# Performance work log

Hardware: AMD Instinct MI355X
Metric: run time of the kernel (lower is better)

## Reference

```python
import jax, jax.numpy as jnp
import numpy as np

NEG = 0.01   # LeakyReLU slope (torch default)
EPS = 1e-5   # BatchNorm1d eps

def lrelu(x):
    return jnp.where(x >= 0, x, NEG * x)

def bn(x, g, b):
    # BatchNorm1d in training mode: biased batch stats
    m = x.mean(0)
    v = x.var(0)
    return g * (x - m) * jax.lax.rsqrt(v + EPS) + b

def gcn_conv(x, edge_index, edge_weight, W, b):
    # PyG GCNConv: add self-loops (weight 1), symmetric normalization, X W then aggregate
    N = x.shape[0]
    loop = jnp.arange(N)
    src = jnp.concatenate([edge_index[0], loop])
    dst = jnp.concatenate([edge_index[1], loop])
    w = jnp.concatenate([edge_weight, jnp.ones((N,), x.dtype)])
    deg = jax.ops.segment_sum(w, dst, num_segments=N)
    dinv = jnp.where(deg > 0, jax.lax.rsqrt(deg), 0.0)
    norm = dinv[src] * w * dinv[dst]            # [E+N]
    h = x @ W                                   # [N, out]
    out = jax.ops.segment_sum(norm[:, None] * h[src], dst, num_segments=N)
    return out + b


def setup_inputs() -> dict:
    key = jax.random.key(0)
    ks = iter(jax.random.split(key, 48))
    B, Nd, Ed, Np_, Ep = 2048, 10000, 65536, 5000, 25000
    D_IN, P_IN, F = 1024, 2812, 300 + 1024 + 1024 + 1024  # F = 3372

    def w(shape):
        return (jax.random.normal(next(ks), shape, jnp.float32) * 0.02)

    inp = {
        'd_index': jax.random.randint(next(ks), (B,), 0, Nd),
        'p_index': jax.random.randint(next(ks), (B,), 0, Np_),
        'd_vecs': jax.random.normal(next(ks), (B, 300), jnp.float32),
        'p_embeddings': jax.random.normal(next(ks), (B, 1024), jnp.float32),
        'd_ecfps': jax.random.normal(next(ks), (Nd, D_IN), jnp.float32),
        'd_edge_index': jax.random.randint(next(ks), (2, Ed), 0, Nd),
        'd_edge_weight': jax.random.uniform(next(ks), (Ed,), jnp.float32),
        'p_gos': jax.random.normal(next(ks), (Np_, P_IN), jnp.float32),
        'p_edge_index': jax.random.randint(next(ks), (2, Ep), 0, Np_),
        'p_edge_weight': jax.random.uniform(next(ks), (Ep,), jnp.float32),
        # GCN params
        'd_gcn_W': w((D_IN, 1024)), 'd_gcn_b': jnp.zeros((1024,), jnp.float32),
        'p_gcn_W': w((P_IN, 1024)), 'p_gcn_b': jnp.zeros((1024,), jnp.float32),
        # encoder
        'enc_W1': w((F, 1024)), 'enc_b1': jnp.zeros((1024,), jnp.float32),
        'enc_g1': jnp.ones((1024,), jnp.float32), 'enc_beta1': jnp.zeros((1024,), jnp.float32),
        'enc_W2': w((1024, 256)), 'enc_b2': jnp.zeros((256,), jnp.float32),
        'enc_g2': jnp.ones((256,), jnp.float32), 'enc_beta2': jnp.zeros((256,), jnp.float32),
        # decoder
        'dec_W1': w((256, 1024)), 'dec_b1': jnp.zeros((1024,), jnp.float32),
        'dec_g1': jnp.ones((1024,), jnp.float32), 'dec_beta1': jnp.zeros((1024,), jnp.float32),
        'dec_W2': w((1024, F)), 'dec_b2': jnp.zeros((F,), jnp.float32),
        'dec_g2': jnp.ones((F,), jnp.float32), 'dec_beta2': jnp.zeros((F,), jnp.float32),
        # output head
        'out_W1': w((256, 64)), 'out_b1': jnp.zeros((64,), jnp.float32),
        'out_g1': jnp.ones((64,), jnp.float32), 'out_beta1': jnp.zeros((64,), jnp.float32),
        'out_W2': w((64, 1)), 'out_b2': jnp.zeros((1,), jnp.float32),
    }
    return inp


def reference(d_index, p_index, d_vecs, p_embeddings, d_ecfps, d_edge_index, d_edge_weight,
              p_gos, p_edge_index, p_edge_weight,
              d_gcn_W, d_gcn_b, p_gcn_W, p_gcn_b,
              enc_W1, enc_b1, enc_g1, enc_beta1, enc_W2, enc_b2, enc_g2, enc_beta2,
              dec_W1, dec_b1, dec_g1, dec_beta1, dec_W2, dec_b2, dec_g2, dec_beta2,
              out_W1, out_b1, out_g1, out_beta1, out_W2, out_b2):
    ecfps = lrelu(gcn_conv(d_ecfps, d_edge_index, d_edge_weight, d_gcn_W, d_gcn_b))[d_index]
    gos = lrelu(gcn_conv(p_gos, p_edge_index, p_edge_weight, p_gcn_W, p_gcn_b))[p_index]
    feature = jnp.concatenate([d_vecs, p_embeddings, ecfps, gos], axis=1)  # [B, 3372]
    h = jax.nn.relu(bn(feature @ enc_W1 + enc_b1, enc_g1, enc_beta1))
    encoded = jax.nn.relu(bn(h @ enc_W2 + enc_b2, enc_g2, enc_beta2))       # [B, 256]
    h = jax.nn.relu(bn(encoded @ dec_W1 + dec_b1, dec_g1, dec_beta1))
    decoded = jax.nn.relu(bn(h @ dec_W2 + dec_b2, dec_g2, dec_beta2))       # [B, 3372]
    h = lrelu(bn(encoded @ out_W1 + out_b1, out_g1, out_beta1))
    y = h @ out_W2 + out_b2                                                  # [B, 1]
    return (y, encoded, decoded, feature)
```

## Files before the change

kernel.cpp:

```cpp
#include <hip/hip_runtime.h>

#define CDIV(a,b) (((a)+(b)-1)/(b))

typedef __attribute__((ext_vector_type(8))) short bf16x8;
typedef __attribute__((ext_vector_type(4))) float f32x4;

__device__ __forceinline__ unsigned short f2b(float v) {
  union { float f; unsigned u; } x; x.f = v;
  unsigned r = x.u + 0x7FFFu + ((x.u >> 16) & 1u);
  return (unsigned short)(r >> 16);
}

__device__ __forceinline__ void gload_lds16(const void* g, void* l) {
  __builtin_amdgcn_global_load_lds(
      (const __attribute__((address_space(1))) unsigned int*)(g),
      (__attribute__((address_space(3))) unsigned int*)(l), 16, 0, 0);
}

struct GA {
  const unsigned short* A;
  const unsigned short* B;
  float* C;
  const int* ridx;
  float* csum;
  float* csumsq;
  int N, K, lda, ldb;
};

__global__ __launch_bounds__(256) void gemm128z(GA g0, GA g1, GA g2, GA g3) {
  __shared__ __align__(16) unsigned short As[2][128 * 64];
  __shared__ __align__(16) unsigned short Bs[2][128 * 64];
  const int z = blockIdx.z;
  GA g = (z == 0) ? g0 : (z == 1) ? g1 : (z == 2) ? g2 : g3;

  const int tid = threadIdx.x;
  const int lane = tid & 63;
  const int wid = tid >> 6;
  const int wm = (wid >> 1) * 64;
  const int wn = (wid & 1) * 64;
  const long bm = (long)blockIdx.x * 128;
  const long bn = (long)blockIdx.y * 128;

  f32x4 acc[4][4] = {};

  const int lr = tid >> 3;
  const int lc = (((tid & 7) ^ (lr & 7)) * 8);

  const unsigned short* ap[4];
  const unsigned short* bp[4];
#pragma unroll
  for (int i = 0; i < 4; ++i) {
    long row = bm + i * 32 + lr;
    long arow = g.ridx ? (long)g.ridx[row] : row;
    ap[i] = g.A + arow * g.lda + lc;
    bp[i] = g.B + (bn + i * 32 + lr) * (long)g.ldb + lc;
  }

  const int rsel = lane & 15;
  const int rx = rsel & 7;

  auto STAGE = [&](int buf, int k0) {
#pragma unroll
    for (int i = 0; i < 4; ++i) {
      const int eoff = (i * 256 + tid) * 8;
      gload_lds16(ap[i] + k0, &As[buf][eoff]);
      gload_lds16(bp[i] + k0, &Bs[buf][eoff]);
    }
  };
  auto COMPUTE = [&](int buf) {
#pragma unroll
    for (int kk = 0; kk < 2; ++kk) {
      const int koz = (((kk * 4 + (lane >> 4)) ^ rx) << 3);
      bf16x8 av[4], bv[4];
#pragma unroll
      for (int m = 0; m < 4; ++m)
        av[m] = *(const bf16x8*)(&As[buf][(wm + m * 16 + rsel) * 64 + koz]);
#pragma unroll
      for (int n = 0; n < 4; ++n)
        bv[n] = *(const bf16x8*)(&Bs[buf][(wn + n * 16 + rsel) * 64 + koz]);
#pragma unroll
      for (int m = 0; m < 4; ++m)
#pragma unroll
        for (int n = 0; n < 4; ++n)
          acc[m][n] = __builtin_amdgcn_mfma_f32_16x16x32_bf16(av[m], bv[n], acc[m][n], 0, 0, 0);
    }
  };

  STAGE(0, 0);
  int cur = 0;
  for (int k0 = 64; k0 < g.K; k0 += 64) {
    STAGE(cur ^ 1, k0);
    asm volatile("s_waitcnt vmcnt(8)" ::: "memory");
    __builtin_amdgcn_s_barrier();
    asm volatile("" ::: "memory");
    COMPUTE(cur);
    asm volatile("" ::: "memory");
    __builtin_amdgcn_s_barrier();
    cur ^= 1;
  }
  asm volatile("s_waitcnt vmcnt(0)" ::: "memory");
  __builtin_amdgcn_s_barrier();
  asm volatile("" ::: "memory");
  COMPUTE(cur);

  const int crow0 = (lane >> 4) * 4;
  const int ccol = lane & 15;
#pragma unroll
  for (int m = 0; m < 4; ++m)
#pragma unroll
    for (int n = 0; n < 4; ++n) {
      const long r = bm + wm + m * 16 + crow0;
      const long c = bn + wn + n * 16 + ccol;
#pragma unroll
      for (int q = 0; q < 4; ++q)
        g.C[(r + q) * (long)g.N + c] = acc[m][n][q];
    }

  if (g.csum) {
#pragma unroll
    for (int n = 0; n < 4; ++n) {
      float s = 0.f, s2 = 0.f;
#pragma unroll
      for (int m = 0; m < 4; ++m)
#pragma unroll
        for (int q = 0; q < 4; ++q) {
          float v = acc[m][n][q];
          s += v; s2 += v * v;
        }
      s  += __shfl_xor(s, 16);  s  += __shfl_xor(s, 32);
      s2 += __shfl_xor(s2, 16); s2 += __shfl_xor(s2, 32);
      if ((lane >> 4) == 0) {
        const long c = bn + wn + n * 16 + ccol;
        atomicAdd(&g.csum[c], s);
        atomicAdd(&g.csumsq[c], s2);
      }
    }
  }
}

__global__ __launch_bounds__(256) void gemm64s(GA g0, GA g1, GA g2, GA g3) {
  __shared__ __align__(16) unsigned short As[2][64 * 64];
  __shared__ __align__(16) unsigned short Bs[2][128 * 64];
  const int z = blockIdx.z;
  GA g = (z == 0) ? g0 : (z == 1) ? g1 : (z == 2) ? g2 : g3;

  const int tid = threadIdx.x;
  const int lane = tid & 63;
  const int wid = tid >> 6;
  const int wn = wid * 32;
  const long bm = (long)blockIdx.x * 64;
  const long bn = (long)blockIdx.y * 128;

  f32x4 acc[4][2] = {};

  const int lr = tid >> 3;
  const int lc = (((tid & 7) ^ (lr & 7)) * 8);

  const long r0 = g.ridx ? (long)g.ridx[bm + lr] : bm + lr;
  const long r1 = g.ridx ? (long)g.ridx[bm + 32 + lr] : bm + 32 + lr;
  const unsigned short* ap0 = g.A + r0 * g.lda + lc;
  const unsigned short* ap1 = g.A + r1 * g.lda + lc;
  const unsigned short* bp0 = g.B + (bn + lr) * (long)g.ldb + lc;
  const unsigned short* bp1 = g.B + (bn + 32 + lr) * (long)g.ldb + lc;
  const unsigned short* bp2 = g.B + (bn + 64 + lr) * (long)g.ldb + lc;
  const unsigned short* bp3 = g.B + (bn + 96 + lr) * (long)g.ldb + lc;

  const int rsel = lane & 15;
  const int rx = rsel & 7;

  auto STAGE = [&](int buf, int k0) {
    gload_lds16(ap0 + k0, &As[buf][tid * 8]);
    gload_lds16(ap1 + k0, &As[buf][(256 + tid) * 8]);
    gload_lds16(bp0 + k0, &Bs[buf][tid * 8]);
    gload_lds16(bp1 + k0, &Bs[buf][(256 + tid) * 8]);
    gload_lds16(bp2 + k0, &Bs[buf][(512 + tid) * 8]);
    gload_lds16(bp3 + k0, &Bs[buf][(768 + tid) * 8]);
  };
  auto COMPUTE = [&](int buf) {
#pragma unroll
    for (int kk = 0; kk < 2; ++kk) {
      const int koz = (((kk * 4 + (lane >> 4)) ^ rx) << 3);
      bf16x8 av[4], bv[2];
#pragma unroll
      for (int m = 0; m < 4; ++m)
        av[m] = *(const bf16x8*)(&As[buf][(m * 16 + rsel) * 64 + koz]);
#pragma unroll
      for (int n = 0; n < 2; ++n)
        bv[n] = *(const bf16x8*)(&Bs[buf][(wn + n * 16 + rsel) * 64 + koz]);
#pragma unroll
      for (int m = 0; m < 4; ++m)
#pragma unroll
        for (int n = 0; n < 2; ++n)
          acc[m][n] = __builtin_amdgcn_mfma_f32_16x16x32_bf16(av[m], bv[n], acc[m][n], 0, 0, 0);
    }
  };

  STAGE(0, 0);
  int cur = 0;
  for (int k0 = 64; k0 < g.K; k0 += 64) {
    STAGE(cur ^ 1, k0);
    asm volatile("s_waitcnt vmcnt(6)" ::: "memory");
    __builtin_amdgcn_s_barrier();
    asm volatile("" ::: "memory");
    COMPUTE(cur);
    asm volatile("" ::: "memory");
    __builtin_amdgcn_s_barrier();
    cur ^= 1;
  }
  asm volatile("s_waitcnt vmcnt(0)" ::: "memory");
  __builtin_amdgcn_s_barrier();
  asm volatile("" ::: "memory");
  COMPUTE(cur);

  const int crow0 = (lane >> 4) * 4;
  const int ccol = lane & 15;
#pragma unroll
  for (int m = 0; m < 4; ++m)
#pragma unroll
    for (int n = 0; n < 2; ++n) {
      const long r = bm + m * 16 + crow0;
      const long c = bn + wn + n * 16 + ccol;
#pragma unroll
      for (int q = 0; q < 4; ++q)
        g.C[(r + q) * (long)g.N + c] = acc[m][n][q];
    }

  if (g.csum) {
#pragma unroll
    for (int n = 0; n < 2; ++n) {
      float s = 0.f, s2 = 0.f;
#pragma unroll
      for (int m = 0; m < 4; ++m)
#pragma unroll
        for (int q = 0; q < 4; ++q) {
          float v = acc[m][n][q];
          s += v; s2 += v * v;
        }
      s  += __shfl_xor(s, 16);  s  += __shfl_xor(s, 32);
      s2 += __shfl_xor(s2, 16); s2 += __shfl_xor(s2, 32);
      if ((lane >> 4) == 0) {
        const long c = bn + wn + n * 16 + ccol;
        atomicAdd(&g.csum[c], s);
        atomicAdd(&g.csumsq[c], s2);
      }
    }
  }
}

__global__ void init_all(int* iz, int nIz, float* deg, int nDeg,
                         float* stats, int nStats) {
  int i = blockIdx.x * 256 + threadIdx.x;
  if (i < nIz) iz[i] = 0;
  if (i < nDeg) deg[i] = 1.f;
  if (i < nStats) stats[i] = 0.f;
}

__global__ void prep_b(const int* __restrict__ d_ei, const float* __restrict__ d_ew,
                       float* __restrict__ deg_d,
                       const int* __restrict__ p_ei, const float* __restrict__ p_ew,
                       float* __restrict__ deg_p,
                       const int* __restrict__ d_index, int* __restrict__ flag_d,
                       const int* __restrict__ p_index, int* __restrict__ flag_p) {
  int e = blockIdx.x * 256 + threadIdx.x;
  if (e < 65536) atomicAdd(&deg_d[d_ei[65536 + e]], d_ew[e]);
  int e2 = e - 65536;
  if (e2 >= 0 && e2 < 25000) atomicAdd(&deg_p[p_ei[25000 + e2]], p_ew[e2]);
  if (e < 2048) flag_d[d_index[e]] = 1;
  else if (e < 4096) flag_p[p_index[e - 2048]] = 1;
}

__global__ void prep_c(float* __restrict__ deg, int nDeg,
                       int* __restrict__ flag_d, int* __restrict__ ctr_d,
                       int* __restrict__ slot_d,
                       int* __restrict__ flag_p, int* __restrict__ ctr_p,
                       int* __restrict__ slot_p) {
  int i = blockIdx.x * 256 + threadIdx.x;
  if (i < nDeg) deg[i] = rsqrtf(deg[i]);
  if (i < 10000) {
    if (flag_d[i]) { int s = atomicAdd(ctr_d, 1); flag_d[i] = s + 1; slot_d[s] = i; }
  } else if (i < 15000) {
    int j = i - 10000;
    if (flag_p[j]) { int s = atomicAdd(ctr_p, 1); flag_p[j] = s + 1; slot_p[s] = j; }
  }
}

__global__ void prep_d(const int* __restrict__ d_index, const int* __restrict__ flag_d,
                       int* __restrict__ ridx_d,
                       const int* __restrict__ p_index, const int* __restrict__ flag_p,
                       int* __restrict__ ridx_p,
                       const int* __restrict__ d_ei, int* __restrict__ cnt_d,
                       const int* __restrict__ p_ei, int* __restrict__ cnt_p) {
  int e = blockIdx.x * 256 + threadIdx.x;
  if (e < 2048) ridx_d[e] = flag_d[d_index[e]] - 1;
  else if (e < 4096) { int j = e - 2048; ridx_p[j] = flag_p[p_index[j]] - 1; }
  if (e < 65536) { int s = flag_d[d_ei[65536 + e]]; if (s) atomicAdd(&cnt_d[s - 1], 1); }
  int e2 = e - 65536;
  if (e2 >= 0 && e2 < 25000) { int s = flag_p[p_ei[25000 + e2]]; if (s) atomicAdd(&cnt_p[s - 1], 1); }
}

__global__ void scan2048x2(const int* __restrict__ cnt_d, int* __restrict__ rp_d,
                           const int* __restrict__ cnt_p, int* __restrict__ rp_p) {
  const int* cnt = blockIdx.x ? cnt_p : cnt_d;
  int* rowptr    = blockIdx.x ? rp_p : rp_d;
  __shared__ int part[256];
  int tid = threadIdx.x;
  int base = tid * 8;
  int vals[8]; int s = 0;
#pragma unroll
  for (int i = 0; i < 8; ++i) { vals[i] = s; s += cnt[base + i]; }
  part[tid] = s;
  __syncthreads();
  if (tid == 0) { int r = 0; for (int i = 0; i < 256; ++i) { int t = part[i]; part[i] = r; r += t; } }
  __syncthreads();
  int off = part[tid];
#pragma unroll
  for (int i = 0; i < 8; ++i) rowptr[base + i] = off + vals[i];
  if (tid == 255) rowptr[2048] = off + s;
}
__global__ void fill_edges2(
    const int* __restrict__ d_ei, const float* __restrict__ d_ew,
    const float* __restrict__ dinv_d, const int* __restrict__ flag_d,
    const int* __restrict__ rp_d, int* __restrict__ fill_d,
    int2* __restrict__ em_d,
    const int* __restrict__ p_ei, const float* __restrict__ p_ew,
    const float* __restrict__ dinv_p, const int* __restrict__ flag_p,
    const int* __restrict__ rp_p, int* __restrict__ fill_p,
    int2* __restrict__ em_p) {
  int e = blockIdx.x * 256 + threadIdx.x;
  if (e < 65536) {
    int dst = d_ei[65536 + e];
    int s = flag_d[dst];
    if (s) {
      int src = d_ei[e];
      int pos = rp_d[s - 1] + atomicAdd(&fill_d[s - 1], 1);
      float cf = d_ew[e] * dinv_d[src] * dinv_d[dst];
      em_d[pos] = make_int2(src, __float_as_int(cf));
    }
  }
  int e2 = e - 65536;
  if (e2 >= 0 && e2 < 25000) {
    int dst = p_ei[25000 + e2];
    int s = flag_p[dst];
    if (s) {
      int src = p_ei[e2];
      int pos = rp_p[s - 1] + atomicAdd(&fill_p[s - 1], 1);
      float cf = p_ew[e2] * dinv_p[src] * dinv_p[dst];
      em_p[pos] = make_int2(src, __float_as_int(cf));
    }
  }
}

__global__ __launch_bounds__(256) void gather_agg5b(
    const float* __restrict__ Xd, const float* __restrict__ dinv_d,
    const int* __restrict__ slot_d, const int* __restrict__ rp_d,
    const int2* __restrict__ em_d,
    const int* __restrict__ nflag_d, unsigned short* __restrict__ aggd,
    const float* __restrict__ Xp, const float* __restrict__ dinv_p,
    const int* __restrict__ slot_p, const int* __restrict__ rp_p,
    const int2* __restrict__ em_p,
    const int* __restrict__ nflag_p, unsigned short* __restrict__ aggp)
{
  const int gw = blockIdx.x * 4 + (threadIdx.x >> 6);
  const int lane = threadIdx.x & 63;

  int slot, c, Kdata4, Kst4, Kld, nflag;
  const float *X, *dinv; const int *slotn, *rp; const int2* em;
  unsigned short* agg;
  if (gw < 8192) {
    slot = gw >> 2;
    c = (gw & 3) * 64 + lane;
    X = Xd; dinv = dinv_d; slotn = slot_d; rp = rp_d; em = em_d;
    nflag = *nflag_d; agg = aggd; Kdata4 = 256; Kst4 = 256; Kld = 1024;
  } else {
    int q = gw - 8192;
    slot = q / 11;
    c = (q - slot * 11) * 64 + lane;
    X = Xp; dinv = dinv_p; slotn = slot_p; rp = rp_p; em = em_p;
    nflag = *nflag_p; agg = aggp; Kdata4 = 703; Kst4 = 704; Kld = 2812;
  }
  if (slot >= nflag) return;

  const int n = slotn[slot];
  const float dn = dinv[n];
  const float selfc = dn * dn;
  const int e0 = rp[slot], e1 = rp[slot + 1];
  const bool valid = c < Kdata4;

  float ax = 0.f, ay = 0.f, az = 0.f, aw = 0.f;
  if (valid) {
    float4 v = *(const float4*)(X + (long)n * Kld + 4 * c);
    ax = selfc * v.x; ay = selfc * v.y; az = selfc * v.z; aw = selfc * v.w;
  }

  int e = e0;
  for (; e + 4 <= e1; e += 4) {
    const int2 m0 = em[e], m1 = em[e + 1], m2 = em[e + 2], m3 = em[e + 3];
    if (valid) {
      float4 v0 = *(const float4*)(X + (long)m0.x * Kld + 4 * c);
      float4 v1 = *(const float4*)(X + (long)m1.x * Kld + 4 * c);
      float4 v2 = *(const float4*)(X + (long)m2.x * Kld + 4 * c);
      float4 v3 = *(const float4*)(X + (long)m3.x * Kld + 4 * c);
      const float c0 = __int_as_float(m0.y), c1 = __int_as_float(m1.y);
      const float c2 = __int_as_float(m2.y), c3 = __int_as_float(m3.y);
      ax += c0 * v0.x; ay += c0 * v0.y; az += c0 * v0.z; aw += c0 * v0.w;
      ax += c1 * v1.x; ay += c1 * v1.y; az += c1 * v1.z; aw += c1 * v1.w;
      ax += c2 * v2.x; ay += c2 * v2.y; az += c2 * v2.z; aw += c2 * v2.w;
      ax += c3 * v3.x; ay += c3 * v3.y; az += c3 * v3.z; aw += c3 * v3.w;
    }
  }
  for (; e < e1; ++e) {
    const int2 m = em[e];
    if (valid) {
      float4 v = *(const float4*)(X + (long)m.x * Kld + 4 * c);
      const float cf = __int_as_float(m.y);
      ax += cf * v.x; ay += cf * v.y; az += cf * v.z; aw += cf * v.w;
    }
  }

  if (c < Kst4) {
    ushort4 o; o.x = f2b(ax); o.y = f2b(ay); o.z = f2b(az); o.w = f2b(aw);
    *(ushort4*)(agg + (long)slot * (Kst4 * 4) + 4 * c) = o;
  }
}

__global__ void transposeAll(
    const float* W0, unsigned short* T0,
    const float* W1, unsigned short* T1,
    const float* W2, unsigned short* T2,
    const float* W3, unsigned short* T3,
    const float* W4, unsigned short* T4,
    const float* W5, unsigned short* T5,
    const float* W6, unsigned short* T6)
{
  __shared__ float tile[32][33];
  int bid = blockIdx.x;
  const float* W; unsigned short* Wt; int K, N, Kp, Np_, tx, local;
  if      (bid <  1024) { W=W0; Wt=T0; K=1024; N=1024; Kp=1024; Np_=1024; tx=32;  local=bid; }
  else if (bid <  3840) { W=W1; Wt=T1; K=2812; N=1024; Kp=2816; Np_=1024; tx=88;  local=bid-1024; }
  else if (bid <  7296) { W=W2; Wt=T2; K=3372; N=1024; Kp=3456; Np_=1024; tx=108; local=bid-3840; }
  else if (bid <  7552) { W=W3; Wt=T3; K=1024; N=256;  Kp=1024; Np_=256;  tx=32;  local=bid-7296; }
  else if (bid <  7808) { W=W4; Wt=T4; K=256;  N=1024; Kp=256;  Np_=1024; tx=8;   local=bid-7552; }
  else if (bid <  7840) { W=W5; Wt=T5; K=256;  N=64;   Kp=256;  Np_=128;  tx=8;   local=bid-7808; }
  else                  { W=W6; Wt=T6; K=1024; N=3372; Kp=1024; Np_=3456; tx=32;  local=bid-7840; }
  int k0 = (local % tx) * 32, n0 = (local / tx) * 32;
  for (int i = threadIdx.y; i < 32; i += 8) {
    int k = k0 + i, n = n0 + threadIdx.x;
    tile[i][threadIdx.x] = (k < K && n < N) ? W[(size_t)k * N + n] : 0.f;
  }
  __syncthreads();
  for (int i = threadIdx.y; i < 32; i += 8) {
    int n = n0 + i, k = k0 + threadIdx.x;
    if (n < Np_ && k < Kp) Wt[(size_t)n * Kp + k] = f2b(tile[threadIdx.x][i]);
  }
}

__global__ void colstats4(const float* __restrict__ Z, const float* __restrict__ Z2,
                          const float* __restrict__ Z3, int ldz, int cols,
                          float* __restrict__ csum, float* __restrict__ csumsq) {
  int c4 = blockIdx.x * 256 + threadIdx.x;
  if (c4 * 4 >= cols) return;
  int r0 = blockIdx.y * 16;
  float sx = 0.f, sy = 0.f, sz_ = 0.f, sw = 0.f;
  float qx = 0.f, qy = 0.f, qz = 0.f, qw = 0.f;
  for (int r = r0; r < r0 + 16; ++r) {
    float4 v = *(const float4*)(Z + (long)r * ldz + 4 * c4);
    if (Z2) { float4 w = *(const float4*)(Z2 + (long)r * ldz + 4 * c4);
              v.x += w.x; v.y += w.y; v.z += w.z; v.w += w.w; }
    if (Z3) { float4 w = *(const float4*)(Z3 + (long)r * ldz + 4 * c4);
              v.x += w.x; v.y += w.y; v.z += w.z; v.w += w.w; }
    sx += v.x; sy += v.y; sz_ += v.z; sw += v.w;
    qx += v.x * v.x; qy += v.y * v.y; qz += v.z * v.z; qw += v.w * v.w;
  }
  atomicAdd(&csum[4 * c4 + 0], sx); atomicAdd(&csum[4 * c4 + 1], sy);
  atomicAdd(&csum[4 * c4 + 2], sz_); atomicAdd(&csum[4 * c4 + 3], sw);
  atomicAdd(&csumsq[4 * c4 + 0], qx); atomicAdd(&csumsq[4 * c4 + 1], qy);
  atomicAdd(&csumsq[4 * c4 + 2], qz); atomicAdd(&csumsq[4 * c4 + 3], qw);
}

__global__ void apply_bn4(const float* __restrict__ Z, const float* __restrict__ Z2,
                          const float* __restrict__ Z3,
                          int ldz, int total4, int cols4,
                          const float* __restrict__ csum, const float* __restrict__ csumsq,
                          const float* __restrict__ g, const float* __restrict__ beta,
                          int leaky,
                          float* __restrict__ f32out, int ldf,
                          unsigned short* __restrict__ b16out, int ldb) {
  int idx = blockIdx.x*256+threadIdx.x;
  if (idx >= total4) return;
  int b = idx / cols4, j = (idx % cols4) * 4;
  float4 v = *(const float4*)(Z + (long)b * ldz + j);
  if (Z2) { float4 w = *(const float4*)(Z2 + (long)b * ldz + j);
            v.x += w.x; v.y += w.y; v.z += w.z; v.w += w.w; }
  if (Z3) { float4 w = *(const float4*)(Z3 + (long)b * ldz + j);
            v.x += w.x; v.y += w.y; v.z += w.z; v.w += w.w; }
  if (csum) {
    const float invB = 1.f / 2048.f;
    float4 cs = *(const float4*)(csum + j);
    float4 cq = *(const float4*)(csumsq + j);
    float4 gg = *(const float4*)(g + j);
    float4 bb = *(const float4*)(beta + j);
    float m, var, sc;
    m = cs.x * invB; var = fmaxf(cq.x * invB - m * m, 0.f);
    sc = gg.x * rsqrtf(var + 1e-5f); v.x = v.x * sc + (bb.x - m * sc);
    m = cs.y * invB; var = fmaxf(cq.y * invB - m * m, 0.f);
    sc = gg.y * rsqrtf(var + 1e-5f); v.y = v.y * sc + (bb.y - m * sc);
    m = cs.z * invB; var = fmaxf(cq.z * invB - m * m, 0.f);
    sc = gg.z * rsqrtf(var + 1e-5f); v.z = v.z * sc + (bb.z - m * sc);
    m = cs.w * invB; var = fmaxf(cq.w * invB - m * m, 0.f);
    sc = gg.w * rsqrtf(var + 1e-5f); v.w = v.w * sc + (bb.w - m * sc);
  } else {
    float4 bb = *(const float4*)(beta + j);
    v.x += bb.x; v.y += bb.y; v.z += bb.z; v.w += bb.w;
  }
  const float neg = leaky ? 0.01f : 0.f;
  v.x = (v.x >= 0.f) ? v.x : neg * v.x;
  v.y = (v.y >= 0.f) ? v.y : neg * v.y;
  v.z = (v.z >= 0.f) ? v.z : neg * v.z;
  v.w = (v.w >= 0.f) ? v.w : neg * v.w;
  if (f32out) *(float4*)(f32out + (long)b * ldf + j) = v;
  if (b16out) {
    ushort4 o; o.x = f2b(v.x); o.y = f2b(v.y); o.z = f2b(v.z); o.w = f2b(v.w);
    *(ushort4*)(b16out + (long)b * ldb + j) = o;
  }
}

__global__ void apply_gcn2(const float* __restrict__ Zd, const float* __restrict__ Pd,
                           const float* __restrict__ bd,
                           const float* __restrict__ Zp, const float* __restrict__ Pp,
                           const float* __restrict__ bp,
                           float* __restrict__ feat_f32, unsigned short* __restrict__ feat_b16) {
  int idx = blockIdx.x*256+threadIdx.x;
  if (idx >= 2 * 2048 * 256) return;
  const bool isP = idx >= 2048 * 256;
  int l = isP ? idx - 2048 * 256 : idx;
  int b = l >> 8, j = (l & 255) * 4;
  const float* Z = isP ? Zp : Zd;
  const float* P = isP ? Pp : Pd;
  const float* bias = isP ? bp : bd;
  const int coloff = isP ? 2348 : 1324;
  float4 v = *(const float4*)(Z + (long)b * 1024 + j);
  float4 w = *(const float4*)(P + (long)b * 1024 + j);
  float4 bb = *(const float4*)(bias + j);
  v.x += w.x + bb.x; v.y += w.y + bb.y; v.z += w.z + bb.z; v.w += w.w + bb.w;
  v.x = (v.x >= 0.f) ? v.x : 0.01f * v.x;
  v.y = (v.y >= 0.f) ? v.y : 0.01f * v.y;
  v.z = (v.z >= 0.f) ? v.z : 0.01f * v.z;
  v.w = (v.w >= 0.f) ? v.w : 0.01f * v.w;
  *(float4*)(feat_f32 + (long)b * 3372 + coloff + j) = v;
  ushort4 o; o.x = f2b(v.x); o.y = f2b(v.y); o.z = f2b(v.z); o.w = f2b(v.w);
  *(ushort4*)(feat_b16 + (long)b * 3456 + coloff + j) = o;
}

__global__ void feat_copy2(const float* __restrict__ dv, const float* __restrict__ pe,
                           float* __restrict__ f32out, unsigned short* __restrict__ b16out) {
  int idx = blockIdx.x*256+threadIdx.x;
  if (idx >= 2048 * 1408) return;
  int b = idx / 1408, c = idx % 1408;
  if (c < 1324) {
    float v = (c < 300) ? dv[b * 300 + c] : pe[(long)b * 1024 + (c - 300)];
    f32out[(long)b * 3372 + c] = v;
    b16out[(long)b * 3456 + c] = f2b(v);
  } else {
    b16out[(long)b * 3456 + 3372 + (c - 1324)] = 0;
  }
}

__global__ void head_fused(const float* __restrict__ Z, int ldz,
                           const float* __restrict__ csum, const float* __restrict__ csumsq,
                           const float* __restrict__ g, const float* __restrict__ beta,
                           const float* __restrict__ W2, const float* __restrict__ b2,
                           float* __restrict__ y) {
  int b = blockIdx.x*256+threadIdx.x;
  if (b >= 2048) return;
  const float invB = 1.f / 2048.f;
  float s = b2[0];
  for (int k = 0; k < 64; ++k) {
    float m = csum[k] * invB;
    float var = fmaxf(csumsq[k] * invB - m * m, 0.f);
    float sc = g[k] * rsqrtf(var + 1e-5f);
    float sh = beta[k] - m * sc;
    float v = Z[(long)b * ldz + k];
    v = v * sc + sh;
    v = (v >= 0.f) ? v : 0.01f * v;
    s += v * W2[k];
  }
  y[b] = s;
}

extern "C" void kernel_launch(void* const* d_in, const int* in_sizes, int n_in,
                              void* d_out, int out_size, void* d_ws, size_t ws_size,
                              hipStream_t stream) {
  (void)in_sizes; (void)n_in; (void)out_size; (void)ws_size;
  const int*   d_index = (const int*)d_in[0];
  const int*   p_index = (const int*)d_in[1];
  const float* d_vecs  = (const float*)d_in[2];
  const float* p_emb   = (const float*)d_in[3];
  const float* d_ecfps = (const float*)d_in[4];
  const int*   d_ei    = (const int*)d_in[5];
  const float* d_ew    = (const float*)d_in[6];
  const float* p_gos   = (const float*)d_in[7];
  const int*   p_ei    = (const int*)d_in[8];
  const float* p_ew    = (const float*)d_in[9];
  const float* d_gcn_W = (const float*)d_in[10];
  const float* d_gcn_b = (const float*)d_in[11];
  const float* p_gcn_W = (const float*)d_in[12];
  const float* p_gcn_b = (const float*)d_in[13];
  const float* enc_W1  = (const float*)d_in[14];
  const float* enc_g1  = (const float*)d_in[16];
  const float* enc_be1 = (const float*)d_in[17];
  const float* enc_W2  = (const float*)d_in[18];
  const float* enc_g2  = (const float*)d_in[20];
  const float* enc_be2 = (const float*)d_in[21];
  const float* dec_W1  = (const float*)d_in[22];
  const float* dec_g1  = (const float*)d_in[24];
  const float* dec_be1 = (const float*)d_in[25];
  const float* dec_W2  = (const float*)d_in[26];
  const float* dec_g2  = (const float*)d_in[28];
  const float* dec_be2 = (const float*)d_in[29];
  const float* out_W1  = (const float*)d_in[30];
  const float* out_g1  = (const float*)d_in[32];
  const float* out_be1 = (const float*)d_in[33];
  const float* out_W2  = (const float*)d_in[34];
  const float* out_b2  = (const float*)d_in[35];

  float* out = (float*)d_out;
  float* y_out    = out;
  float* enc_out  = out + 2048;
  float* dec_out  = out + 526336;
  float* feat_out = out + 7432192;

  char* ws = (char*)d_ws;
  size_t off = 0;
  auto alloc = [&](size_t bytes) {
    size_t o = off; off = (off + bytes + 255) & ~(size_t)255; return (void*)(ws + o);
  };
  int* iz = (int*)alloc((size_t)23194 * 4);
  int* flag_d = iz;
  int* flag_p = iz + 10000;
  int* cnt_d  = iz + 15000;
  int* cnt_p  = iz + 17048;
  int* fill_d = iz + 19096;
  int* fill_p = iz + 21144;
  int* ctr    = iz + 23192;
  int* slotnode_d = (int*)alloc(2048 * 4);
  int* slotnode_p = (int*)alloc(2048 * 4);
  int* rowptr_d = (int*)alloc(2049 * 4);
  int* rowptr_p = (int*)alloc(2049 * 4);
  int* ridx_d = (int*)alloc(2048 * 4);
  int* ridx_p = (int*)alloc(2048 * 4);
  int2* em_d = (int2*)alloc((size_t)65536 * 8);
  int2* em_p = (int2*)alloc((size_t)25000 * 8);
  float* deg   = (float*)alloc((size_t)15000 * 4);
  float* deg_d = deg;
  float* deg_p = deg + 10000;
  float* stats = (float*)alloc((size_t)34560 * 4);
  float* cs_e1 = stats,         * cq_e1 = stats + 3456;
  float* cs_e2 = stats + 6912,  * cq_e2 = stats + 10368;
  float* cs_d1 = stats + 13824, * cq_d1 = stats + 17280;
  float* cs_d2 = stats + 27648, * cq_d2 = stats + 31104;
  unsigned short* aggd_b = (unsigned short*)alloc((size_t)2048 * 1024 * 2);
  unsigned short* aggp_b = (unsigned short*)alloc((size_t)2048 * 2816 * 2);
  unsigned short* WdT   = (unsigned short*)alloc((size_t)1024 * 1024 * 2);
  unsigned short* WpT   = (unsigned short*)alloc((size_t)1024 * 2816 * 2);
  unsigned short* eW1T  = (unsigned short*)alloc((size_t)1024 * 3456 * 2);
  unsigned short* eW2T  = (unsigned short*)alloc((size_t)256 * 1024 * 2);
  unsigned short* dhT   = (unsigned short*)alloc((size_t)1152 * 256 * 2);
  unsigned short* dW2T  = (unsigned short*)alloc((size_t)3456 * 1024 * 2);
  unsigned short* featb = (unsigned short*)alloc((size_t)2048 * 3456 * 2);
  float* Z    = (float*)alloc((size_t)2048 * 3456 * 4);
  float* P0   = (float*)alloc((size_t)2048 * 1152 * 4);
  float* P1   = (float*)alloc((size_t)2048 * 1152 * 4);
  float* P2   = (float*)alloc((size_t)2048 * 1152 * 4);
  unsigned short* h1b  = (unsigned short*)alloc((size_t)2048 * 1024 * 2);
  unsigned short* encb = (unsigned short*)alloc((size_t)2048 * 256 * 2);
  unsigned short* h3b  = (unsigned short*)alloc((size_t)2048 * 1024 * 2);

  init_all<<<CDIV(34560,256),256,0,stream>>>(iz, 23194, deg, 15000, stats, 34560);
  prep_b<<<CDIV(90536,256),256,0,stream>>>(d_ei, d_ew, deg_d, p_ei, p_ew, deg_p,
                                           d_index, flag_d, p_index, flag_p);
  prep_c<<<CDIV(15000,256),256,0,stream>>>(deg, 15000, flag_d, ctr, slotnode_d,
                                           flag_p, ctr + 1, slotnode_p);
  prep_d<<<CDIV(90536,256),256,0,stream>>>(d_index, flag_d, ridx_d, p_index, flag_p, ridx_p,
                                           d_ei, cnt_d, p_ei, cnt_p);
  scan2048x2<<<2,256,0,stream>>>(cnt_d, rowptr_d, cnt_p, rowptr_p);
  fill_edges2<<<CDIV(90536,256),256,0,stream>>>(
      d_ei, d_ew, deg_d, flag_d, rowptr_d, fill_d, em_d,
      p_ei, p_ew, deg_p, flag_p, rowptr_p, fill_p, em_p);
  gather_agg5b<<<7680,256,0,stream>>>(
      d_ecfps, deg_d, slotnode_d, rowptr_d, em_d, ctr, aggd_b,
      p_gos,   deg_p, slotnode_p, rowptr_p, em_p, ctr + 1, aggp_b);

  transposeAll<<<11296, dim3(32,8), 0, stream>>>(
      d_gcn_W, WdT, p_gcn_W, WpT, enc_W1, eW1T, enc_W2, eW2T,
      dec_W1, dhT, out_W1, dhT + (size_t)1024 * 256, dec_W2, dW2T);

  {
    GA gd0{aggd_b,        WdT,        Z,  ridx_d, nullptr, nullptr, 1024,  512, 1024, 1024};
    GA gd1{aggd_b + 512,  WdT + 512,  P0, ridx_d, nullptr, nullptr, 1024,  512, 1024, 1024};
    GA gp0{aggp_b,        WpT,        P1, ridx_p, nullptr, nullptr, 1024, 1408, 2816, 2816};
    GA gp1{aggp_b + 1408, WpT + 1408, P2, ridx_p, nullptr, nullptr, 1024, 1408, 2816, 2816};
    gemm128z<<<dim3(16,8,4),256,0,stream>>>(gd0, gd1, gp0, gp1);
  }
  apply_gcn2<<<CDIV(2*2048*256,256),256,0,stream>>>(Z, P0, d_gcn_b, P1, P2, p_gcn_b,
                                                    feat_out, featb);
  feat_copy2<<<CDIV(2048*1408,256),256,0,stream>>>(d_vecs, p_emb, feat_out, featb);

  {
    GA e0{featb,        eW1T,        Z,  nullptr, nullptr, nullptr, 1024, 1152, 3456, 3456};
    GA e1{featb + 1152, eW1T + 1152, P0, nullptr, nullptr, nullptr, 1024, 1152, 3456, 3456};
    GA e2{featb + 2304, eW1T + 2304, P1, nullptr, nullptr, nullptr, 1024, 1152, 3456, 3456};
    gemm128z<<<dim3(16,8,3),256,0,stream>>>(e0, e1, e2, e0);
  }
  colstats4<<<dim3(1,128),256,0,stream>>>(Z, P0, P1, 1024, 1024, cs_e1, cq_e1);
  apply_bn4<<<CDIV(2048*256,256),256,0,stream>>>(Z, P0, P1, 1024, 2048*256, 256,
      cs_e1, cq_e1, enc_g1, enc_be1, 0, nullptr, 0, h1b, 1024);

  {
    GA e0{h1b,       eW2T,       Z,  nullptr, nullptr, nullptr, 256, 512, 1024, 1024};
    GA e1{h1b + 512, eW2T + 512, P0, nullptr, nullptr, nullptr, 256, 512, 1024, 1024};
    gemm64s<<<dim3(32,2,2),256,0,stream>>>(e0, e1, e0, e0);
  }
  colstats4<<<dim3(1,128),256,0,stream>>>(Z, P0, nullptr, 256, 256, cs_e2, cq_e2);
  apply_bn4<<<CDIV(2048*64,256),256,0,stream>>>(Z, P0, nullptr, 256, 2048*64, 64,
      cs_e2, cq_e2, enc_g2, enc_be2, 0, enc_out, 256, encb, 256);

  {
    GA g0{encb, dhT, Z, nullptr, cs_d1, cq_d1, 1152, 256, 256, 256};
    gemm64s<<<dim3(32,9,1),256,0,stream>>>(g0, g0, g0, g0);
  }
  apply_bn4<<<CDIV(2048*256,256),256,0,stream>>>(Z, nullptr, nullptr, 1152, 2048*256, 256,
      cs_d1, cq_d1, dec_g1, dec_be1, 0, nullptr, 0, h3b, 1024);
  head_fused<<<8,256,0,stream>>>(Z + 1024, 1152, cs_d1 + 1024, cq_d1 + 1024,
                                 out_g1, out_be1, out_W2, out_b2, y_out);

  {
    GA g0{h3b, dW2T, Z, nullptr, cs_d2, cq_d2, 3456, 1024, 1024, 1024};
    gemm128z<<<dim3(16,27,1),256,0,stream>>>(g0, g0, g0, g0);
  }
  apply_bn4<<<CDIV(2048*843,256),256,0,stream>>>(Z, nullptr, nullptr, 3456, 2048*843, 843,
      cs_d2, cq_d2, dec_g2, dec_be2, 0, dec_out, 3372, nullptr, 0);
}
```

Baseline: 291.0 us.

## Fuse final decoder GEMM with batchnorm via grid barrier; merge feature kernels

The last decoder GEMM now computes column statistics, waits at a global atomic-counter barrier until all 432 blocks finish, then applies batchnorm and ReLU straight from registers into the output. This drops the fp32 intermediate write and reread plus a separate apply_bn launch. The two feature-assembly kernels are also merged into one vectorized kernel. The grid barrier depends on all 432 blocks being co-resident, and the epilogue writes are strided per column (uncoalesced).

```diff
diff --git a/kernel.cpp b/kernel.cpp
--- a/kernel.cpp
+++ b/kernel.cpp
@@ -133,6 +133,138 @@
         const long c = bn + wn + n * 16 + ccol;
         atomicAdd(&g.csum[c], s);
         atomicAdd(&g.csumsq[c], s2);
+      }
+    }
+  }
+}
+
+__global__ __launch_bounds__(256) void gemm128_bn(
+    GA g, const float* __restrict__ gamma, const float* __restrict__ beta,
+    float* __restrict__ outp, int outN, int nblocks, int* __restrict__ done_ctr) {
+  __shared__ __align__(16) unsigned short As[2][128 * 64];
+  __shared__ __align__(16) unsigned short Bs[2][128 * 64];
+
+  const int tid = threadIdx.x;
+  const int lane = tid & 63;
+  const int wid = tid >> 6;
+  const int wm = (wid >> 1) * 64;
+  const int wn = (wid & 1) * 64;
+  const long bm = (long)blockIdx.x * 128;
+  const long bn = (long)blockIdx.y * 128;
+
+  f32x4 acc[4][4] = {};
+
+  const int lr = tid >> 3;
+  const int lc = (((tid & 7) ^ (lr & 7)) * 8);
+
+  const unsigned short* ap[4];
+  const unsigned short* bp[4];
+#pragma unroll
+  for (int i = 0; i < 4; ++i) {
+    long row = bm + i * 32 + lr;
+    ap[i] = g.A + row * g.lda + lc;
+    bp[i] = g.B + (bn + i * 32 + lr) * (long)g.ldb + lc;
+  }
+
+  const int rsel = lane & 15;
+  const int rx = rsel & 7;
+
+  auto STAGE = [&](int buf, int k0) {
+#pragma unroll
+    for (int i = 0; i < 4; ++i) {
+      const int eoff = (i * 256 + tid) * 8;
+      gload_lds16(ap[i] + k0, &As[buf][eoff]);
+      gload_lds16(bp[i] + k0, &Bs[buf][eoff]);
+    }
+  };
+  auto COMPUTE = [&](int buf) {
+#pragma unroll
+    for (int kk = 0; kk < 2; ++kk) {
+      const int koz = (((kk * 4 + (lane >> 4)) ^ rx) << 3);
+      bf16x8 av[4], bv[4];
+#pragma unroll
+      for (int m = 0; m < 4; ++m)
+        av[m] = *(const bf16x8*)(&As[buf][(wm + m * 16 + rsel) * 64 + koz]);
+#pragma unroll
+      for (int n = 0; n < 4; ++n)
+        bv[n] = *(const bf16x8*)(&Bs[buf][(wn + n * 16 + rsel) * 64 + koz]);
+#pragma unroll
+      for (int m = 0; m < 4; ++m)
+#pragma unroll
+        for (int n = 0; n < 4; ++n)
+          acc[m][n] = __builtin_amdgcn_mfma_f32_16x16x32_bf16(av[m], bv[n], acc[m][n], 0, 0, 0);
+    }
+  };
+
+  STAGE(0, 0);
+  int cur = 0;
+  for (int k0 = 64; k0 < g.K; k0 += 64) {
+    STAGE(cur ^ 1, k0);
+    asm volatile("s_waitcnt vmcnt(8)" ::: "memory");
+    __builtin_amdgcn_s_barrier();
+    asm volatile("" ::: "memory");
+    COMPUTE(cur);
+    asm volatile("" ::: "memory");
+    __builtin_amdgcn_s_barrier();
+    cur ^= 1;
+  }
+  asm volatile("s_waitcnt vmcnt(0)" ::: "memory");
+  __builtin_amdgcn_s_barrier();
+  asm volatile("" ::: "memory");
+  COMPUTE(cur);
+
+  const int crow0 = (lane >> 4) * 4;
+  const int ccol = lane & 15;
+
+#pragma unroll
+  for (int n = 0; n < 4; ++n) {
+    float s = 0.f, s2 = 0.f;
+#pragma unroll
+    for (int m = 0; m < 4; ++m)
+#pragma unroll
+      for (int q = 0; q < 4; ++q) {
+        float v = acc[m][n][q];
+        s += v; s2 += v * v;
+      }
+    s  += __shfl_xor(s, 16);  s  += __shfl_xor(s, 32);
+    s2 += __shfl_xor(s2, 16); s2 += __shfl_xor(s2, 32);
+    if ((lane >> 4) == 0) {
+      const long c = bn + wn + n * 16 + ccol;
+      atomicAdd(&g.csum[c], s);
+      atomicAdd(&g.csumsq[c], s2);
+    }
+  }
+
+  __threadfence();
+  __syncthreads();
+  if (tid == 0) {
+    atomicAdd(done_ctr, 1);
+    while (__hip_atomic_load(done_ctr, __ATOMIC_ACQUIRE,
+                             __HIP_MEMORY_SCOPE_AGENT) < nblocks) {
+      __builtin_amdgcn_s_sleep(8);
+    }
+  }
+  __syncthreads();
+
+  const float invB = 1.f / 2048.f;
+#pragma unroll
+  for (int n = 0; n < 4; ++n) {
+    const long c = bn + wn + n * 16 + ccol;
+    if (c >= outN) continue;
+    float cs = __hip_atomic_load(&g.csum[c], __ATOMIC_RELAXED, __HIP_MEMORY_SCOPE_AGENT);
+    float cq = __hip_atomic_load(&g.csumsq[c], __ATOMIC_RELAXED, __HIP_MEMORY_SCOPE_AGENT);
+    float m_ = cs * invB;
+    float var = fmaxf(cq * invB - m_ * m_, 0.f);
+    float sc = gamma[c] * rsqrtf(var + 1e-5f);
+    float sh = beta[c] - m_ * sc;
+#pragma unroll
+    for (int m = 0; m < 4; ++m) {
+      const long r = bm + wm + m * 16 + crow0;
+#pragma unroll
+      for (int q = 0; q < 4; ++q) {
+        float v = acc[m][n][q] * sc + sh;
+        v = (v >= 0.f) ? v : 0.f;
+        outp[(r + q) * (long)outN + c] = v;
       }
     }
   }
@@ -524,44 +656,50 @@
   }
 }
 
-__global__ void apply_gcn2(const float* __restrict__ Zd, const float* __restrict__ Pd,
+__global__ void apply_feat(const float* __restrict__ Zd, const float* __restrict__ Pd,
                            const float* __restrict__ bd,
                            const float* __restrict__ Zp, const float* __restrict__ Pp,
                            const float* __restrict__ bp,
+                           const float* __restrict__ dv, const float* __restrict__ pe,
                            float* __restrict__ feat_f32, unsigned short* __restrict__ feat_b16) {
   int idx = blockIdx.x*256+threadIdx.x;
-  if (idx >= 2 * 2048 * 256) return;
-  const bool isP = idx >= 2048 * 256;
-  int l = isP ? idx - 2048 * 256 : idx;
-  int b = l >> 8, j = (l & 255) * 4;
-  const float* Z = isP ? Zp : Zd;
-  const float* P = isP ? Pp : Pd;
-  const float* bias = isP ? bp : bd;
-  const int coloff = isP ? 2348 : 1324;
-  float4 v = *(const float4*)(Z + (long)b * 1024 + j);
-  float4 w = *(const float4*)(P + (long)b * 1024 + j);
-  float4 bb = *(const float4*)(bias + j);
-  v.x += w.x + bb.x; v.y += w.y + bb.y; v.z += w.z + bb.z; v.w += w.w + bb.w;
-  v.x = (v.x >= 0.f) ? v.x : 0.01f * v.x;
-  v.y = (v.y >= 0.f) ? v.y : 0.01f * v.y;
-  v.z = (v.z >= 0.f) ? v.z : 0.01f * v.z;
-  v.w = (v.w >= 0.f) ? v.w : 0.01f * v.w;
-  *(float4*)(feat_f32 + (long)b * 3372 + coloff + j) = v;
-  ushort4 o; o.x = f2b(v.x); o.y = f2b(v.y); o.z = f2b(v.z); o.w = f2b(v.w);
-  *(ushort4*)(feat_b16 + (long)b * 3456 + coloff + j) = o;
-}
-
-__global__ void feat_copy2(const float* __restrict__ dv, const float* __restrict__ pe,
-                           float* __restrict__ f32out, unsigned short* __restrict__ b16out) {
-  int idx = blockIdx.x*256+threadIdx.x;
-  if (idx >= 2048 * 1408) return;
-  int b = idx / 1408, c = idx % 1408;
-  if (c < 1324) {
-    float v = (c < 300) ? dv[b * 300 + c] : pe[(long)b * 1024 + (c - 300)];
-    f32out[(long)b * 3372 + c] = v;
-    b16out[(long)b * 3456 + c] = f2b(v);
+  const int APPLY_N = 2 * 2048 * 256;
+  if (idx < APPLY_N) {
+    const bool isP = idx >= 2048 * 256;
+    int l = isP ? idx - 2048 * 256 : idx;
+    int b = l >> 8, j = (l & 255) * 4;
+    const float* Z = isP ? Zp : Zd;
+    const float* P = isP ? Pp : Pd;
+    const float* bias = isP ? bp : bd;
+    const int coloff = isP ? 2348 : 1324;
+    float4 v = *(const float4*)(Z + (long)b * 1024 + j);
+    float4 w = *(const float4*)(P + (long)b * 1024 + j);
+    float4 bb = *(const float4*)(bias + j);
+    v.x += w.x + bb.x; v.y += w.y + bb.y; v.z += w.z + bb.z; v.w += w.w + bb.w;
+    v.x = (v.x >= 0.f) ? v.x : 0.01f * v.x;
+    v.y = (v.y >= 0.f) ? v.y : 0.01f * v.y;
+    v.z = (v.z >= 0.f) ? v.z : 0.01f * v.z;
+    v.w = (v.w >= 0.f) ? v.w : 0.01f * v.w;
+    *(float4*)(feat_f32 + (long)b * 3372 + coloff + j) = v;
+    ushort4 o; o.x = f2b(v.x); o.y = f2b(v.y); o.z = f2b(v.z); o.w = f2b(v.w);
+    *(ushort4*)(feat_b16 + (long)b * 3456 + coloff + j) = o;
+    return;
+  }
+  int q = idx - APPLY_N;
+  if (q >= 2048 * 352) return;
+  int b = q / 352, u = q % 352;
+  if (u < 331) {
+    int c = u * 4;
+    float4 v;
+    if (u < 75) v = *(const float4*)(dv + (long)b * 300 + c);
+    else        v = *(const float4*)(pe + (long)b * 1024 + (c - 300));
+    *(float4*)(feat_f32 + (long)b * 3372 + c) = v;
+    ushort4 o; o.x = f2b(v.x); o.y = f2b(v.y); o.z = f2b(v.z); o.w = f2b(v.w);
+    *(ushort4*)(feat_b16 + (long)b * 3456 + c) = o;
   } else {
-    b16out[(long)b * 3456 + 3372 + (c - 1324)] = 0;
+    int c = 3372 + (u - 331) * 4;
+    ushort4 o; o.x = 0; o.y = 0; o.z = 0; o.w = 0;
+    *(ushort4*)(feat_b16 + (long)b * 3456 + c) = o;
   }
 }
 
@@ -634,7 +772,7 @@
   auto alloc = [&](size_t bytes) {
     size_t o = off; off = (off + bytes + 255) & ~(size_t)255; return (void*)(ws + o);
   };
-  int* iz = (int*)alloc((size_t)23194 * 4);
+  int* iz = (int*)alloc((size_t)23200 * 4);
   int* flag_d = iz;
   int* flag_p = iz + 10000;
   int* cnt_d  = iz + 15000;
@@ -642,6 +780,7 @@
   int* fill_d = iz + 19096;
   int* fill_p = iz + 21144;
   int* ctr    = iz + 23192;
+  int* done_ctr = iz + 23196;
   int* slotnode_d = (int*)alloc(2048 * 4);
   int* slotnode_p = (int*)alloc(2048 * 4);
   int* rowptr_d = (int*)alloc(2049 * 4);
@@ -675,7 +814,7 @@
   unsigned short* encb = (unsigned short*)alloc((size_t)2048 * 256 * 2);
   unsigned short* h3b  = (unsigned short*)alloc((size_t)2048 * 1024 * 2);
 
-  init_all<<<CDIV(34560,256),256,0,stream>>>(iz, 23194, deg, 15000, stats, 34560);
+  init_all<<<CDIV(34560,256),256,0,stream>>>(iz, 23200, deg, 15000, stats, 34560);
   prep_b<<<CDIV(90536,256),256,0,stream>>>(d_ei, d_ew, deg_d, p_ei, p_ew, deg_p,
                                            d_index, flag_d, p_index, flag_p);
   prep_c<<<CDIV(15000,256),256,0,stream>>>(deg, 15000, flag_d, ctr, slotnode_d,
@@ -701,9 +840,8 @@
     GA gp1{aggp_b + 1408, WpT + 1408, P2, ridx_p, nullptr, nullptr, 1024, 1408, 2816, 2816};
     gemm128z<<<dim3(16,8,4),256,0,stream>>>(gd0, gd1, gp0, gp1);
   }
-  apply_gcn2<<<CDIV(2*2048*256,256),256,0,stream>>>(Z, P0, d_gcn_b, P1, P2, p_gcn_b,
-                                                    feat_out, featb);
-  feat_copy2<<<CDIV(2048*1408,256),256,0,stream>>>(d_vecs, p_emb, feat_out, featb);
+  apply_feat<<<CDIV(2*2048*256 + 2048*352,256),256,0,stream>>>(
+      Z, P0, d_gcn_b, P1, P2, p_gcn_b, d_vecs, p_emb, feat_out, featb);
 
   {
     GA e0{featb,        eW1T,        Z,  nullptr, nullptr, nullptr, 1024, 1152, 3456, 3456};
@@ -734,9 +872,8 @@
                                  out_g1, out_be1, out_W2, out_b2, y_out);
 
   {
-    GA g0{h3b, dW2T, Z, nullptr, cs_d2, cq_d2, 3456, 1024, 1024, 1024};
-    gemm128z<<<dim3(16,27,1),256,0,stream>>>(g0, g0, g0, g0);
-  }
-  apply_bn4<<<CDIV(2048*843,256),256,0,stream>>>(Z, nullptr, nullptr, 3456, 2048*843, 843,
-      cs_d2, cq_d2, dec_g2, dec_be2, 0, dec_out, 3372, nullptr, 0);
-}
+    GA g0{h3b, dW2T, nullptr, nullptr, cs_d2, cq_d2, 3456, 1024, 1024, 1024};
+    gemm128_bn<<<dim3(16,27),256,0,stream>>>(g0, dec_g2, dec_be2, dec_out, 3372,
+                                             432, done_ctr);
+  }
+}
```

Result: slower. 338.4 us (+16.3%).
